# Optimization experiments

Hardware: AMD Instinct MI355X
Metric: run time of the kernel (lower is better)

## Reference

```python
import jax, jax.numpy as jnp
import numpy as np

N, M, L = 16384, 4096, 8
GAMMA = 1.0


def setup_inputs() -> dict:
    key = jax.random.key(0)
    ks = jax.random.split(key, 10)
    layer_W = jax.random.normal(ks[0], (L, 2, 2), jnp.float32)
    layer_b = jax.random.normal(ks[1], (L, 2), jnp.float32)
    # clip=True for all layers after the input layer (construction-time clamp)
    layer_W = layer_W.at[1:].set(jnp.clip(layer_W[1:], -5.0, 5.0))
    layer_b = layer_b.at[1:].set(jnp.clip(layer_b[1:], -5.0, 5.0))
    return {
        "x": jax.random.normal(ks[2], (N, 2), jnp.float32),
        "layer_W": layer_W,
        "layer_b": layer_b,
        "layer_scale": jax.random.normal(ks[3], (L, 2), jnp.float32),
        "layer_shift": jax.random.normal(ks[4], (L, 2), jnp.float32),
        "reference_set": jax.random.normal(ks[5], (M, 2), jnp.float32),
        "W1": jax.random.normal(ks[6], (4, 1), jnp.float32),
        "b1": jax.random.normal(ks[7], (4,), jnp.float32),
        "W2": jax.random.normal(ks[8], (2, 4), jnpp if False else jnp.float32),
        "b2": jax.random.normal(ks[9], (2,), jnp.float32),
    }


def _phi(z):
    # quantum-inspired feature map: [..., 2] -> [..., 4]
    return jnp.concatenate([jnp.sin(z), jnp.cos(z)], axis=-1)


def reference(x, layer_W, layer_b, layer_scale, layer_shift, reference_set, W1, b1, W2, b2):
    # chained tiny layers: tanh(linear(h)) * scale + shift
    def step(h, params):
        W, b, s, t = params
        return jnp.tanh(h @ W.T + b) * s + t, None

    feats, _ = jax.lax.scan(step, x, (layer_W, layer_b, layer_scale, layer_shift))  # [N,2]

    a = _phi(feats)            # [N,4]
    bref = _phi(reference_set)  # [M,4]
    # ||a-b||^2 = ||a||^2 + ||b||^2 - 2 a.b  (avoids [N,M,4] diff tensor)
    dist_sq = (
        jnp.sum(a * a, axis=-1)[:, None]
        + jnp.sum(bref * bref, axis=-1)[None, :]
        - 2.0 * (a @ bref.T)
    )  # [N,M]
    k = jnp.exp(-GAMMA * dist_sq)
    aggregated = jnp.mean(k, axis=1, keepdims=True)  # [N,1]
    h = jnp.tanh(aggregated @ W1.T + b1)  # [N,4]
    logits = h @ W2.T + b2                # [N,2]
    return jax.nn.softmax(logits, axis=-1)
```

## Files before the change

kernel.cpp:

```cpp
#include <hip/hip_runtime.h>

#define NROWS 16384
#define MREF 4096
#define NLAYER 8
#define BLOCK 256

#define RPT 4
#define MCHUNK 128
#define MCHUNKS (MREF / MCHUNK)
#define NSEG (NROWS / RPT)

#define WS_SUMS 0
#define WS_ROWC (NROWS)
#define WS_REFC (NROWS + NROWS * 4)


__global__ __launch_bounds__(BLOCK) void prep(
    const float* __restrict__ x,
    const float* __restrict__ layer_W,
    const float* __restrict__ layer_b,
    const float* __restrict__ layer_scale,
    const float* __restrict__ layer_shift,
    const float* __restrict__ refset,
    float* __restrict__ ws)
{
    const int n = blockIdx.x * BLOCK + threadIdx.x;

    ws[WS_SUMS + n] = 0.0f;

    float h0 = x[n * 2 + 0];
    float h1 = x[n * 2 + 1];
#pragma unroll
    for (int l = 0; l < NLAYER; ++l) {
        const float w00 = layer_W[l * 4 + 0];
        const float w01 = layer_W[l * 4 + 1];
        const float w10 = layer_W[l * 4 + 2];
        const float w11 = layer_W[l * 4 + 3];
        const float b0 = layer_b[l * 2 + 0];
        const float b1 = layer_b[l * 2 + 1];
        const float s0 = layer_scale[l * 2 + 0];
        const float s1 = layer_scale[l * 2 + 1];
        const float t0 = layer_shift[l * 2 + 0];
        const float t1 = layer_shift[l * 2 + 1];
        const float n0 = fmaf(tanhf(fmaf(h1, w01, fmaf(h0, w00, b0))), s0, t0);
        const float n1 = fmaf(tanhf(fmaf(h1, w11, fmaf(h0, w10, b1))), s1, t1);
        h0 = n0; h1 = n1;
    }

    float sf0, cf0, sf1, cf1;
    sincosf(h0, &sf0, &cf0);
    sincosf(h1, &sf1, &cf1);

    const float L2E2 = 2.0f * 1.4426950408889634f;
    float4* rowc = (float4*)(ws + WS_SUMS) + WS_ROWC / 4;
    rowc = (float4*)&ws[NROWS];
    float4 rc; rc.x = sf0 * L2E2; rc.y = sf1 * L2E2; rc.z = cf0 * L2E2; rc.w = cf1 * L2E2;
    rowc[n] = rc;

    if (n < MREF) {
        const float r0 = refset[n * 2 + 0];
        const float r1 = refset[n * 2 + 1];
        float s0, c0, s1, c1;
        sincosf(r0, &s0, &c0);
        sincosf(r1, &s1, &c1);
        float4* refc = (float4*)&ws[WS_REFC];
        float4 v; v.x = s0; v.y = s1; v.z = c0; v.w = c1;
        refc[n] = v;
    }
}

__global__ __launch_bounds__(BLOCK) void pair_sum(float* __restrict__ ws)
{
    __shared__ float4 sref[MCHUNK];

    const int tid = threadIdx.x;
    const int mbase = blockIdx.y * MCHUNK;

    const float4* __restrict__ refc = (const float4*)&ws[WS_REFC];
    const float4* __restrict__ rowc = (const float4*)&ws[NROWS];
    float* __restrict__ sums = ws + WS_SUMS;

    if (tid < MCHUNK) sref[tid] = refc[mbase + tid];

    const int base = blockIdx.x * BLOCK + tid;

    float4 c0 = rowc[base + 0 * NSEG];
    float4 c1 = rowc[base + 1 * NSEG];
    float4 c2 = rowc[base + 2 * NSEG];
    float4 c3 = rowc[base + 3 * NSEG];

    __syncthreads();

    float a0 = 0.0f, a1 = 0.0f, a2 = 0.0f, a3 = 0.0f;
#pragma unroll 4
    for (int i = 0; i < MCHUNK; ++i) {
        const float4 v = sref[i];
        float d0 = c0.x * v.x; d0 = fmaf(c0.y, v.y, d0); d0 = fmaf(c0.z, v.z, d0); d0 = fmaf(c0.w, v.w, d0);
        float d1 = c1.x * v.x; d1 = fmaf(c1.y, v.y, d1); d1 = fmaf(c1.z, v.z, d1); d1 = fmaf(c1.w, v.w, d1);
        float d2 = c2.x * v.x; d2 = fmaf(c2.y, v.y, d2); d2 = fmaf(c2.z, v.z, d2); d2 = fmaf(c2.w, v.w, d2);
        float d3 = c3.x * v.x; d3 = fmaf(c3.y, v.y, d3); d3 = fmaf(c3.z, v.z, d3); d3 = fmaf(c3.w, v.w, d3);
        a0 += exp2f(d0);
        a1 += exp2f(d1);
        a2 += exp2f(d2);
        a3 += exp2f(d3);
    }

    atomicAdd(&sums[base + 0 * NSEG], a0);
    atomicAdd(&sums[base + 1 * NSEG], a1);
    atomicAdd(&sums[base + 2 * NSEG], a2);
    atomicAdd(&sums[base + 3 * NSEG], a3);
}

__global__ __launch_bounds__(BLOCK) void epilogue(
    const float* __restrict__ ws,
    const float* __restrict__ W1,
    const float* __restrict__ b1,
    const float* __restrict__ W2,
    const float* __restrict__ b2,
    float* __restrict__ out)
{
    const int n = blockIdx.x * BLOCK + threadIdx.x;
    const float C = 1.8315638888734179e-2f / (float)MREF;
    const float agg = ws[WS_SUMS + n] * C;

    float h[4];
#pragma unroll
    for (int j = 0; j < 4; ++j) {
        h[j] = tanhf(fmaf(agg, W1[j], b1[j]));
    }
    float l0 = b2[0], l1 = b2[1];
#pragma unroll
    for (int j = 0; j < 4; ++j) {
        l0 = fmaf(W2[0 * 4 + j], h[j], l0);
        l1 = fmaf(W2[1 * 4 + j], h[j], l1);
    }
    const float mx = fmaxf(l0, l1);
    const float e0 = __expf(l0 - mx);
    const float e1 = __expf(l1 - mx);
    const float inv = 1.0f / (e0 + e1);
    out[2 * n + 0] = e0 * inv;
    out[2 * n + 1] = e1 * inv;
}

extern "C" void kernel_launch(void* const* d_in, const int* in_sizes, int n_in,
                              void* d_out, int out_size, void* d_ws, size_t ws_size,
                              hipStream_t stream) {
    const float* x           = (const float*)d_in[0];
    const float* layer_W     = (const float*)d_in[1];
    const float* layer_b     = (const float*)d_in[2];
    const float* layer_scale = (const float*)d_in[3];
    const float* layer_shift = (const float*)d_in[4];
    const float* refset      = (const float*)d_in[5];
    const float* W1          = (const float*)d_in[6];
    const float* b1          = (const float*)d_in[7];
    const float* W2          = (const float*)d_in[8];
    const float* b2          = (const float*)d_in[9];
    float* out = (float*)d_out;
    float* ws  = (float*)d_ws;

    prep<<<NROWS / BLOCK, BLOCK, 0, stream>>>(x, layer_W, layer_b, layer_scale,
                                              layer_shift, refset, ws);

    dim3 grid(NSEG / BLOCK, MCHUNKS);
    pair_sum<<<grid, BLOCK, 0, stream>>>(ws);

    epilogue<<<NROWS / BLOCK, BLOCK, 0, stream>>>(ws, W1, b1, W2, b2, out);
}
```

Baseline: 98.32 us.

## Fuse epilogue into pair_sum via last-block partial-sum reduction

Replaces per-row atomicAdd accumulation and the separate epilogue kernel with per-chunk partial-sum stores plus a per-segment arrival counter. The last block to finish for each row segment reduces all partials and applies the MLP and softmax directly. This removes one kernel launch and the float atomics, at the cost of extra partial-buffer traffic, thread fences, and a serialized tail reduction in the last block per segment.

```diff
diff --git a/kernel.cpp b/kernel.cpp
--- a/kernel.cpp
+++ b/kernel.cpp
@@ -9,10 +9,12 @@
 #define MCHUNK 128
 #define MCHUNKS (MREF / MCHUNK)
 #define NSEG (NROWS / RPT)
+#define SEGS (NSEG / BLOCK)
 
-#define WS_SUMS 0
-#define WS_ROWC (NROWS)
-#define WS_REFC (NROWS + NROWS * 4)
+#define WS_ROWC 0
+#define WS_REFC (NROWS * 4)
+#define WS_PART (NROWS * 4 + MREF * 4)
+#define WS_CNT  (WS_PART + MCHUNKS * NSEG * 4)
 
 
 __global__ __launch_bounds__(BLOCK) void prep(
@@ -26,7 +28,7 @@
 {
     const int n = blockIdx.x * BLOCK + threadIdx.x;
 
-    ws[WS_SUMS + n] = 0.0f;
+    if (n < SEGS) ((int*)&ws[WS_CNT])[n] = 0;
 
     float h0 = x[n * 2 + 0];
     float h1 = x[n * 2 + 1];
@@ -52,8 +54,7 @@
     sincosf(h1, &sf1, &cf1);
 
     const float L2E2 = 2.0f * 1.4426950408889634f;
-    float4* rowc = (float4*)(ws + WS_SUMS) + WS_ROWC / 4;
-    rowc = (float4*)&ws[NROWS];
+    float4* rowc = (float4*)&ws[WS_ROWC];
     float4 rc; rc.x = sf0 * L2E2; rc.y = sf1 * L2E2; rc.z = cf0 * L2E2; rc.w = cf1 * L2E2;
     rowc[n] = rc;
 
@@ -69,20 +70,30 @@
     }
 }
 
-__global__ __launch_bounds__(BLOCK) void pair_sum(float* __restrict__ ws)
+__global__ __launch_bounds__(BLOCK) void pair_sum(
+    float* __restrict__ ws,
+    const float* __restrict__ W1,
+    const float* __restrict__ b1,
+    const float* __restrict__ W2,
+    const float* __restrict__ b2,
+    float* __restrict__ out)
 {
     __shared__ float4 sref[MCHUNK];
+    __shared__ bool amLast;
 
     const int tid = threadIdx.x;
-    const int mbase = blockIdx.y * MCHUNK;
+    const int seg = blockIdx.x;
+    const int y = blockIdx.y;
+    const int mbase = y * MCHUNK;
 
     const float4* __restrict__ refc = (const float4*)&ws[WS_REFC];
-    const float4* __restrict__ rowc = (const float4*)&ws[NROWS];
-    float* __restrict__ sums = ws + WS_SUMS;
+    const float4* __restrict__ rowc = (const float4*)&ws[WS_ROWC];
+    float4* __restrict__ part = (float4*)&ws[WS_PART];
+    int* __restrict__ cnt = (int*)&ws[WS_CNT];
 
     if (tid < MCHUNK) sref[tid] = refc[mbase + tid];
 
-    const int base = blockIdx.x * BLOCK + tid;
+    const int base = seg * BLOCK + tid;
 
     float4 c0 = rowc[base + 0 * NSEG];
     float4 c1 = rowc[base + 1 * NSEG];
@@ -105,41 +116,50 @@
         a3 += exp2f(d3);
     }
 
-    atomicAdd(&sums[base + 0 * NSEG], a0);
-    atomicAdd(&sums[base + 1 * NSEG], a1);
-    atomicAdd(&sums[base + 2 * NSEG], a2);
-    atomicAdd(&sums[base + 3 * NSEG], a3);
-}
+    float4 mine; mine.x = a0; mine.y = a1; mine.z = a2; mine.w = a3;
+    part[y * NSEG + base] = mine;
 
-__global__ __launch_bounds__(BLOCK) void epilogue(
-    const float* __restrict__ ws,
-    const float* __restrict__ W1,
-    const float* __restrict__ b1,
-    const float* __restrict__ W2,
-    const float* __restrict__ b2,
-    float* __restrict__ out)
-{
-    const int n = blockIdx.x * BLOCK + threadIdx.x;
-    const float C = 1.8315638888734179e-2f / (float)MREF;
-    const float agg = ws[WS_SUMS + n] * C;
+    __threadfence();
+    __syncthreads();
+    if (tid == 0) {
+        const int old = atomicAdd(&cnt[seg], 1);
+        amLast = (old == MCHUNKS - 1);
+    }
+    __syncthreads();
 
-    float h[4];
+    if (amLast) {
+        __threadfence();
+        float4 s; s.x = 0.0f; s.y = 0.0f; s.z = 0.0f; s.w = 0.0f;
 #pragma unroll
-    for (int j = 0; j < 4; ++j) {
-        h[j] = tanhf(fmaf(agg, W1[j], b1[j]));
+        for (int y2 = 0; y2 < MCHUNKS; ++y2) {
+            const float4 p = part[y2 * NSEG + base];
+            s.x += p.x; s.y += p.y; s.z += p.z; s.w += p.w;
+        }
+
+        const float C = 1.8315638888734179e-2f / (float)MREF;
+        const float w1_0 = W1[0], w1_1 = W1[1], w1_2 = W1[2], w1_3 = W1[3];
+        const float b1_0 = b1[0], b1_1 = b1[1], b1_2 = b1[2], b1_3 = b1[3];
+        const float agg[RPT] = { s.x * C, s.y * C, s.z * C, s.w * C };
+#pragma unroll
+        for (int j = 0; j < RPT; ++j) {
+            const float h0 = tanhf(fmaf(agg[j], w1_0, b1_0));
+            const float h1 = tanhf(fmaf(agg[j], w1_1, b1_1));
+            const float h2 = tanhf(fmaf(agg[j], w1_2, b1_2));
+            const float h3 = tanhf(fmaf(agg[j], w1_3, b1_3));
+            float l0 = b2[0], l1 = b2[1];
+            l0 = fmaf(W2[0], h0, l0); l0 = fmaf(W2[1], h1, l0);
+            l0 = fmaf(W2[2], h2, l0); l0 = fmaf(W2[3], h3, l0);
+            l1 = fmaf(W2[4], h0, l1); l1 = fmaf(W2[5], h1, l1);
+            l1 = fmaf(W2[6], h2, l1); l1 = fmaf(W2[7], h3, l1);
+            const float mx = fmaxf(l0, l1);
+            const float e0 = __expf(l0 - mx);
+            const float e1 = __expf(l1 - mx);
+            const float inv = 1.0f / (e0 + e1);
+            const int row = base + j * NSEG;
+            out[2 * row + 0] = e0 * inv;
+            out[2 * row + 1] = e1 * inv;
+        }
     }
-    float l0 = b2[0], l1 = b2[1];
-#pragma unroll
-    for (int j = 0; j < 4; ++j) {
-        l0 = fmaf(W2[0 * 4 + j], h[j], l0);
-        l1 = fmaf(W2[1 * 4 + j], h[j], l1);
-    }
-    const float mx = fmaxf(l0, l1);
-    const float e0 = __expf(l0 - mx);
-    const float e1 = __expf(l1 - mx);
-    const float inv = 1.0f / (e0 + e1);
-    out[2 * n + 0] = e0 * inv;
-    out[2 * n + 1] = e1 * inv;
 }
 
 extern "C" void kernel_launch(void* const* d_in, const int* in_sizes, int n_in,
@@ -161,8 +181,6 @@
     prep<<<NROWS / BLOCK, BLOCK, 0, stream>>>(x, layer_W, layer_b, layer_scale,
                                               layer_shift, refset, ws);
 
-    dim3 grid(NSEG / BLOCK, MCHUNKS);
-    pair_sum<<<grid, BLOCK, 0, stream>>>(ws);
-
-    epilogue<<<NROWS / BLOCK, BLOCK, 0, stream>>>(ws, W1, b1, W2, b2, out);
+    dim3 grid(SEGS, MCHUNKS);
+    pair_sum<<<grid, BLOCK, 0, stream>>>(ws, W1, b1, W2, b2, out);
 }
```

Measured after the change: 135.8 us. 38.2% more time.
